# Kernel tuning notes

Measured on AMD Instinct MI355X. Metric: run time of the kernel, lower is better.

## Reference

```python
import jax, jax.numpy as jnp
import numpy as np

M, K, N = 8192, 4096, 16384


def setup_inputs() -> dict:
    key = jax.random.key(0)
    k1, k2 = jax.random.split(key)
    x = jax.random.normal(k1, (M, K), dtype=jnp.float32)
    weight = jax.random.normal(k2, (N, K), dtype=jnp.float32) * 0.02  # reset_parameters: std=0.02
    bias = jnp.zeros((N,), dtype=jnp.float32)
    return {"input": x, "weight": weight, "bias": bias}


def _pow2_scale(amax):
    # round_scale=True: round the dynamic scale up to a power of two
    s = jnp.maximum(amax / 127.0, 1e-30)
    return jnp.exp2(jnp.ceil(jnp.log2(s)))


def _smooth_quant(x):
    # per-row dynamic int8 quantization of an already-smoothed matrix
    amax = jnp.max(jnp.abs(x), axis=-1, keepdims=True)  # [rows, 1]
    scale = _pow2_scale(amax)
    q = jnp.clip(jnp.round(x / scale), -127.0, 127.0)  # int8 values held in f32
    return q, scale


def reference(input, weight, bias):
    # smooth_scale = sqrt(colwise absmax(x) * colwise absmax(W)), shape [K]
    input_maxs = jnp.max(jnp.abs(input), axis=0)
    weight_maxs = jnp.max(jnp.abs(weight), axis=0)
    smooth_scale = jnp.sqrt(input_maxs * weight_maxs)

    x_q, x_scale = _smooth_quant(input / smooth_scale)   # [M,K], [M,1]
    w_q, w_scale = _smooth_quant(weight * smooth_scale)  # [N,K], [N,1]

    # _scaled_mm: (x_q @ w_q.T) * x_scale[:,None] * w_scale[None,:]
    out = jnp.einsum('mk,nk->mn', x_q, w_q) * x_scale * w_scale.T
    out = out + bias
    return out
```

## Files before the change

kernel.cpp:

```cpp
#include <hip/hip_runtime.h>
#include <hip/hip_bf16.h>

typedef __attribute__((ext_vector_type(4))) int i32x4;

__device__ inline float pow2_ceil(float s) {
    unsigned u = __float_as_uint(s);
    if ((u & 0x007fffffu) == 0) return s;
    return __uint_as_float(((u >> 23) + 1) << 23);
}

__global__ __launch_bounds__(256) void colmax_kernel(
    const float* __restrict__ src, int K, float* __restrict__ out)
{
    int col = (blockIdx.x * 256 + threadIdx.x) * 4;
    const float* p = src + (size_t)blockIdx.y * 64 * K + col;
    float mx = 0.f, my = 0.f, mz = 0.f, mw = 0.f;
    for (int r = 0; r < 64; ++r) {
        float4 v = *(const float4*)p;
        mx = fmaxf(mx, fabsf(v.x));
        my = fmaxf(my, fabsf(v.y));
        mz = fmaxf(mz, fabsf(v.z));
        mw = fmaxf(mw, fabsf(v.w));
        p += K;
    }
    atomicMax((unsigned int*)(out + col + 0), __float_as_uint(mx));
    atomicMax((unsigned int*)(out + col + 1), __float_as_uint(my));
    atomicMax((unsigned int*)(out + col + 2), __float_as_uint(mz));
    atomicMax((unsigned int*)(out + col + 3), __float_as_uint(mw));
}

__global__ __launch_bounds__(256) void smooth_kernel(
    const float* __restrict__ xmax, const float* __restrict__ wmax,
    float* __restrict__ smooth, int K)
{
    int i = blockIdx.x * 256 + threadIdx.x;
    if (i < K) smooth[i] = sqrtf(xmax[i] * wmax[i]);
}

template <bool MUL>
__global__ __launch_bounds__(256) void quant_kernel(
    const float* __restrict__ src, const float* __restrict__ smooth,
    signed char* __restrict__ q, float* __restrict__ scale_out, int K)
{
    __shared__ float red[4];
    const int row = blockIdx.x;
    const int tid = threadIdx.x;
    const float* sr = src + (size_t)row * K;

    float v[16];
    float amax = 0.f;
#pragma unroll
    for (int c = 0; c < 4; ++c) {
        int idx = (c << 10) + (tid << 2);
        float4 xv = *(const float4*)(sr + idx);
        float4 sv = *(const float4*)(smooth + idx);
        float a, b, cc, d;
        if (MUL) { a = xv.x * sv.x; b = xv.y * sv.y; cc = xv.z * sv.z; d = xv.w * sv.w; }
        else     { a = xv.x / sv.x; b = xv.y / sv.y; cc = xv.z / sv.z; d = xv.w / sv.w; }
        v[c*4+0] = a; v[c*4+1] = b; v[c*4+2] = cc; v[c*4+3] = d;
        amax = fmaxf(amax, fmaxf(fmaxf(fabsf(a), fabsf(b)), fmaxf(fabsf(cc), fabsf(d))));
    }
#pragma unroll
    for (int off = 32; off > 0; off >>= 1)
        amax = fmaxf(amax, __shfl_down(amax, off, 64));
    if ((tid & 63) == 0) red[tid >> 6] = amax;
    __syncthreads();
    float m = fmaxf(fmaxf(red[0], red[1]), fmaxf(red[2], red[3]));

    float s = fmaxf(m / 127.0f, 1e-30f);
    float scale = pow2_ceil(s);
    if (tid == 0) scale_out[row] = scale;
    float inv = 1.0f / scale;

#pragma unroll
    for (int c = 0; c < 4; ++c) {
        char4 o;
        o.x = (signed char)(int)fminf(fmaxf(rintf(v[c*4+0] * inv), -127.f), 127.f);
        o.y = (signed char)(int)fminf(fmaxf(rintf(v[c*4+1] * inv), -127.f), 127.f);
        o.z = (signed char)(int)fminf(fmaxf(rintf(v[c*4+2] * inv), -127.f), 127.f);
        o.w = (signed char)(int)fminf(fmaxf(rintf(v[c*4+3] * inv), -127.f), 127.f);
        *(char4*)(q + (size_t)row * K + (c << 10) + (tid << 2)) = o;
    }
}

#define G2L(g, l) __builtin_amdgcn_global_load_lds( \
    (const __attribute__((address_space(1))) unsigned char*)(g), \
    (__attribute__((address_space(3))) unsigned char*)(l), 16, 0, 0)

__global__ __launch_bounds__(512, 2) void gemm_i8_256(
    const signed char* __restrict__ Aq, const signed char* __restrict__ Bq,
    const float* __restrict__ xs, const float* __restrict__ wsc,
    const float* __restrict__ bias, float* __restrict__ out,
    int M, int N, int K)
{
    __shared__ signed char lds[131072];

    const int tid = threadIdx.x;

    const int nbx = gridDim.x;
    int lid = blockIdx.y * nbx + blockIdx.x;
    const int nwg = nbx * gridDim.y;
    const int q8 = nwg >> 3, r8 = nwg & 7;
    const int xcd = lid & 7, idx = lid >> 3;
    lid = (xcd < r8 ? xcd * (q8 + 1) : r8 * (q8 + 1) + (xcd - r8) * q8) + idx;
    const int bm = lid / nbx, bn = lid % nbx;

    const int lane = tid & 63;
    const int wave = tid >> 6;
    const int r16 = lane & 15, quad = lane >> 4;
    const int wr = wave >> 2;
    const int wc = wave & 3;

    const signed char* Ab = Aq + (size_t)(bm * 256) * K;
    const signed char* Bb = Bq + (size_t)(bn * 256) * K;

    const int srow  = tid >> 2;
    const int sslot = tid & 3;
    const int gslot = ((sslot ^ (srow & 3)) << 4);
    const size_t arow0 = (size_t)srow * K;
    const size_t arow1 = (size_t)(srow + 128) * K;
    const int sdst = tid << 4;

    const int sw   = (quad ^ (r16 & 3)) << 4;
    const int aoff = ((wr * 128 + r16) << 6) + sw;
    const int boff = 65536 + ((wc * 64 + r16) << 6) + sw;

    i32x4 acc[8][4] = {};
    const int NT = K >> 7;

    G2L(Ab + arow0 + gslot,              lds + sdst);
    G2L(Ab + arow1 + gslot,              lds + 8192 + sdst);
    G2L(Bb + arow0 + gslot,              lds + 65536 + sdst);
    G2L(Bb + arow1 + gslot,              lds + 65536 + 8192 + sdst);
    G2L(Ab + arow0 + 64 + gslot,         lds + 16384 + sdst);
    G2L(Ab + arow1 + 64 + gslot,         lds + 16384 + 8192 + sdst);
    G2L(Bb + arow0 + 64 + gslot,         lds + 65536 + 16384 + sdst);
    G2L(Bb + arow1 + 64 + gslot,         lds + 65536 + 16384 + 8192 + sdst);
    asm volatile("s_waitcnt vmcnt(4)" ::: "memory");
    __builtin_amdgcn_s_barrier();

    for (int t = 0; t < NT; ++t) {
        const int bofs  = (t & 1) << 15;
        const int nbofs = bofs ^ 32768;
        const size_t kc = (size_t)((t + 1 < NT) ? (t + 1) : t) << 7;
        i32x4 af[4], bf[4];

#pragma unroll
        for (int mi = 0; mi < 4; ++mi)
            af[mi] = *(const i32x4*)(lds + bofs + aoff + mi * 1024);
#pragma unroll
        for (int ni = 0; ni < 4; ++ni)
            bf[ni] = *(const i32x4*)(lds + bofs + boff + ni * 1024);
        G2L(Ab + arow0 + kc + gslot, lds + nbofs + sdst);
        G2L(Ab + arow1 + kc + gslot, lds + nbofs + 8192 + sdst);
        __builtin_amdgcn_s_barrier();
        __builtin_amdgcn_s_setprio(1);
#pragma unroll
        for (int mi = 0; mi < 4; ++mi)
#pragma unroll
            for (int ni = 0; ni < 4; ++ni)
                acc[mi][ni] = __builtin_amdgcn_mfma_i32_16x16x64_i8(af[mi], bf[ni], acc[mi][ni], 0, 0, 0);
        __builtin_amdgcn_s_setprio(0);
        __builtin_amdgcn_s_barrier();

#pragma unroll
        for (int mi = 0; mi < 4; ++mi)
            af[mi] = *(const i32x4*)(lds + bofs + aoff + 4096 + mi * 1024);
        G2L(Bb + arow0 + kc + gslot, lds + nbofs + 65536 + sdst);
        G2L(Bb + arow1 + kc + gslot, lds + nbofs + 65536 + 8192 + sdst);
        asm volatile("s_waitcnt vmcnt(4)" ::: "memory");
        __builtin_amdgcn_s_barrier();
        __builtin_amdgcn_s_setprio(1);
#pragma unroll
        for (int mi = 0; mi < 4; ++mi)
#pragma unroll
            for (int ni = 0; ni < 4; ++ni)
                acc[mi + 4][ni] = __builtin_amdgcn_mfma_i32_16x16x64_i8(af[mi], bf[ni], acc[mi + 4][ni], 0, 0, 0);
        __builtin_amdgcn_s_setprio(0);
        __builtin_amdgcn_s_barrier();

#pragma unroll
        for (int mi = 0; mi < 4; ++mi)
            af[mi] = *(const i32x4*)(lds + bofs + aoff + 16384 + mi * 1024);
#pragma unroll
        for (int ni = 0; ni < 4; ++ni)
            bf[ni] = *(const i32x4*)(lds + bofs + boff + 16384 + ni * 1024);
        G2L(Ab + arow0 + kc + 64 + gslot, lds + nbofs + 16384 + sdst);
        G2L(Ab + arow1 + kc + 64 + gslot, lds + nbofs + 16384 + 8192 + sdst);
        __builtin_amdgcn_s_barrier();
        __builtin_amdgcn_s_setprio(1);
#pragma unroll
        for (int mi = 0; mi < 4; ++mi)
#pragma unroll
            for (int ni = 0; ni < 4; ++ni)
                acc[mi][ni] = __builtin_amdgcn_mfma_i32_16x16x64_i8(af[mi], bf[ni], acc[mi][ni], 0, 0, 0);
        __builtin_amdgcn_s_setprio(0);
        __builtin_amdgcn_s_barrier();

#pragma unroll
        for (int mi = 0; mi < 4; ++mi)
            af[mi] = *(const i32x4*)(lds + bofs + aoff + 16384 + 4096 + mi * 1024);
        G2L(Bb + arow0 + kc + 64 + gslot, lds + nbofs + 65536 + 16384 + sdst);
        G2L(Bb + arow1 + kc + 64 + gslot, lds + nbofs + 65536 + 16384 + 8192 + sdst);
        asm volatile("s_waitcnt vmcnt(4)" ::: "memory");
        __builtin_amdgcn_s_barrier();
        __builtin_amdgcn_s_setprio(1);
#pragma unroll
        for (int mi = 0; mi < 4; ++mi)
#pragma unroll
            for (int ni = 0; ni < 4; ++ni)
                acc[mi + 4][ni] = __builtin_amdgcn_mfma_i32_16x16x64_i8(af[mi], bf[ni], acc[mi + 4][ni], 0, 0, 0);
        __builtin_amdgcn_s_setprio(0);
        __builtin_amdgcn_s_barrier();
    }

#pragma unroll
    for (int ni = 0; ni < 4; ++ni) {
        int gn = bn * 256 + wc * 64 + ni * 16 + r16;
        float wv = wsc[gn];
        float bv = bias[gn];
#pragma unroll
        for (int mi = 0; mi < 8; ++mi) {
#pragma unroll
            for (int i = 0; i < 4; ++i) {
                int gm = bm * 256 + wr * 128 + mi * 16 + quad * 4 + i;
                out[(size_t)gm * N + gn] = (float)acc[mi][ni][i] * xs[gm] * wv + bv;
            }
        }
    }
}

extern "C" void kernel_launch(void* const* d_in, const int* in_sizes, int n_in,
                              void* d_out, int out_size, void* d_ws, size_t ws_size,
                              hipStream_t stream)
{
    const float* x    = (const float*)d_in[0];
    const float* w    = (const float*)d_in[1];
    const float* bias = (const float*)d_in[2];
    float* out = (float*)d_out;

    const int N = in_sizes[2];
    const int K = in_sizes[1] / N;
    const int M = in_sizes[0] / K;

    float* xmax   = (float*)d_ws;
    float* wmax   = xmax + K;
    float* smooth = wmax + K;
    float* xscale = smooth + K;
    float* wscale = xscale + M;
    signed char* xq = (signed char*)(wscale + N);
    signed char* wq = xq + (size_t)M * K;

    hipMemsetAsync(xmax, 0, (size_t)2 * K * sizeof(float), stream);

    colmax_kernel<<<dim3(K / 1024, M / 64), 256, 0, stream>>>(x, K, xmax);
    colmax_kernel<<<dim3(K / 1024, N / 64), 256, 0, stream>>>(w, K, wmax);
    smooth_kernel<<<dim3((K + 255) / 256), 256, 0, stream>>>(xmax, wmax, smooth, K);
    quant_kernel<false><<<dim3(M), 256, 0, stream>>>(x, smooth, xq, xscale, K);
    quant_kernel<true ><<<dim3(N), 256, 0, stream>>>(w, smooth, wq, wscale, K);
    gemm_i8_256<<<dim3(N / 256, M / 256), 512, 0, stream>>>(
        xq, wq, xscale, wscale, bias, out, M, N, K);
}
```

Baseline: 1.418 ms.

## Merge column-max kernels, unroll loads, and change LDS swizzle pattern

```diff
diff --git a/kernel.cpp b/kernel.cpp
--- a/kernel.cpp
+++ b/kernel.cpp
@@ -9,24 +9,35 @@
     return __uint_as_float(((u >> 23) + 1) << 23);
 }
 
-__global__ __launch_bounds__(256) void colmax_kernel(
-    const float* __restrict__ src, int K, float* __restrict__ out)
-{
+__global__ __launch_bounds__(256) void colmax2_kernel(
+    const float* __restrict__ x, const float* __restrict__ w,
+    int K, int xblocks, float* __restrict__ xmax, float* __restrict__ wmax)
+{
+    const int by = blockIdx.y;
+    const float* src;
+    float* out;
+    if (by < xblocks) { src = x + (size_t)by * 32 * K;            out = xmax; }
+    else              { src = w + (size_t)(by - xblocks) * 32 * K; out = wmax; }
+
     int col = (blockIdx.x * 256 + threadIdx.x) * 4;
-    const float* p = src + (size_t)blockIdx.y * 64 * K + col;
-    float mx = 0.f, my = 0.f, mz = 0.f, mw = 0.f;
-    for (int r = 0; r < 64; ++r) {
-        float4 v = *(const float4*)p;
-        mx = fmaxf(mx, fabsf(v.x));
-        my = fmaxf(my, fabsf(v.y));
-        mz = fmaxf(mz, fabsf(v.z));
-        mw = fmaxf(mw, fabsf(v.w));
-        p += K;
-    }
-    atomicMax((unsigned int*)(out + col + 0), __float_as_uint(mx));
-    atomicMax((unsigned int*)(out + col + 1), __float_as_uint(my));
-    atomicMax((unsigned int*)(out + col + 2), __float_as_uint(mz));
-    atomicMax((unsigned int*)(out + col + 3), __float_as_uint(mw));
+    const float* p = src + col;
+    float m0 = 0.f, m1 = 0.f, m2 = 0.f, m3 = 0.f;
+#pragma unroll
+    for (int r = 0; r < 32; r += 4) {
+        float4 a = *(const float4*)(p);
+        float4 b = *(const float4*)(p + K);
+        float4 c = *(const float4*)(p + 2 * (size_t)K);
+        float4 d = *(const float4*)(p + 3 * (size_t)K);
+        p += 4 * (size_t)K;
+        m0 = fmaxf(fmaxf(m0, fabsf(a.x)), fmaxf(fmaxf(fabsf(b.x), fabsf(c.x)), fabsf(d.x)));
+        m1 = fmaxf(fmaxf(m1, fabsf(a.y)), fmaxf(fmaxf(fabsf(b.y), fabsf(c.y)), fabsf(d.y)));
+        m2 = fmaxf(fmaxf(m2, fabsf(a.z)), fmaxf(fmaxf(fabsf(b.z), fabsf(c.z)), fabsf(d.z)));
+        m3 = fmaxf(fmaxf(m3, fabsf(a.w)), fmaxf(fmaxf(fabsf(b.w), fabsf(c.w)), fabsf(d.w)));
+    }
+    atomicMax((unsigned int*)(out + col + 0), __float_as_uint(m0));
+    atomicMax((unsigned int*)(out + col + 1), __float_as_uint(m1));
+    atomicMax((unsigned int*)(out + col + 2), __float_as_uint(m2));
+    atomicMax((unsigned int*)(out + col + 3), __float_as_uint(m3));
 }
 
 __global__ __launch_bounds__(256) void smooth_kernel(
@@ -116,12 +127,12 @@
 
     const int srow  = tid >> 2;
     const int sslot = tid & 3;
-    const int gslot = ((sslot ^ (srow & 3)) << 4);
+    const int gslot = ((sslot ^ ((srow >> 1) & 3)) << 4);
     const size_t arow0 = (size_t)srow * K;
     const size_t arow1 = (size_t)(srow + 128) * K;
     const int sdst = tid << 4;
 
-    const int sw   = (quad ^ (r16 & 3)) << 4;
+    const int sw   = (quad ^ ((r16 >> 1) & 3)) << 4;
     const int aoff = ((wr * 128 + r16) << 6) + sw;
     const int boff = 65536 + ((wc * 64 + r16) << 6) + sw;
 
@@ -253,8 +264,9 @@
 
     hipMemsetAsync(xmax, 0, (size_t)2 * K * sizeof(float), stream);
 
-    colmax_kernel<<<dim3(K / 1024, M / 64), 256, 0, stream>>>(x, K, xmax);
-    colmax_kernel<<<dim3(K / 1024, N / 64), 256, 0, stream>>>(w, K, wmax);
+    const int xblocks = M / 32;
+    colmax2_kernel<<<dim3(K / 1024, xblocks + N / 32), 256, 0, stream>>>(
+        x, w, K, xblocks, xmax, wmax);
     smooth_kernel<<<dim3((K + 255) / 256), 256, 0, stream>>>(xmax, wmax, smooth, K);
     quant_kernel<false><<<dim3(M), 256, 0, stream>>>(x, smooth, xq, xscale, K);
     quant_kernel<true ><<<dim3(N), 256, 0, stream>>>(w, smooth, wq, wscale, K);
```

Result: no change. 1.393 ms (-1.8%).
